# Kernel tuning notes

Measured on AMD Instinct MI355X. Metric: run time of the kernel, lower is better.

The kernel has to match this reference:

```python
import jax, jax.numpy as jnp
import numpy as np

TAU_RC = 0.02
TAU_REF = 0.002
V_TH = 1.0
EPS = 1e-7


def lif_rate(I):
    # LIF firing-rate nonlinearity: r = 1/(tau_ref - tau_rc*log1p(-v_th/I)) for I > v_th+eps else 0
    good = I > V_TH + EPS
    safe_I = jnp.where(good, I, V_TH + 1.0)  # avoid log1p of invalid values
    r = 1.0 / (TAU_REF - TAU_RC * jnp.log1p(-V_TH / safe_I))
    return jnp.where(good, r, 0.0)


def setup_inputs() -> dict:
    key = jax.random.key(0)
    kq, kk, kv, ke, kg, kb = jax.random.split(key, 6)
    B, H, T, D = 2, 16, 2048, 64
    block_size = 2048
    Q = jax.random.normal(kq, (B, H, T, D), dtype=jnp.float32)
    K = jax.random.normal(kk, (B, H, T, D), dtype=jnp.float32)
    V = jax.random.normal(kv, (B, H, T, D), dtype=jnp.float32)
    enc = jax.random.normal(ke, (H, block_size, D), dtype=jnp.float32)
    # F.normalize(enc, dim=-1, eps=1e-8): x / max(||x||, eps)
    norm = jnp.maximum(jnp.linalg.norm(enc, axis=-1, keepdims=True), 1e-8)
    enc_hat = enc / norm
    gain = jax.random.uniform(kg, (1, H, block_size, 1), dtype=jnp.float32) * 200.0
    bias = jax.random.uniform(kb, (1, H, block_size, 1), dtype=jnp.float32)
    return {"Q": Q, "K": K, "V": V, "enc_hat": enc_hat, "gain": gain, "bias": bias}


def reference(Q, K, V, enc_hat, gain, bias):
    B, H, T, D = Q.shape
    temperature = jnp.asarray(D ** 0.5, dtype=Q.dtype)
    E = enc_hat[:, :T, :]          # [H, T, D]
    G = gain[:, :, :T, :]          # [1, H, T, 1]
    BIAS = bias[:, :, :T, :]       # [1, H, T, 1]
    # scores against fixed encoders (K is unused, matching the original module)
    I = G * jnp.einsum('bhtd,hsd->bhts', Q, E) + BIAS   # [B, H, T, T]
    scores = lif_rate(I) / temperature
    causal = jnp.tril(jnp.ones((T, T), dtype=bool))[None, None]
    scores = jnp.where(causal, scores, -jnp.inf)
    attn = jax.nn.softmax(scores, axis=-1)
    return jnp.einsum('bhts,bhsd->bhtd', attn, V)
```

## Files before the change

### kernel.cpp

```cpp
#include <hip/hip_runtime.h>
#include <hip/hip_bf16.h>
#include <math.h>

constexpr int Bb = 2, Hh = 16, Tt = 2048;

typedef __attribute__((ext_vector_type(8))) _Float16 f16x8;
typedef __attribute__((ext_vector_type(8))) short bf16x8;
typedef __attribute__((ext_vector_type(4))) float f32x4;
typedef __attribute__((ext_vector_type(16))) float f32x16;
typedef __attribute__((ext_vector_type(4))) short short4v;
typedef unsigned int u32;

__device__ __forceinline__ short f2bf(float x){ __hip_bfloat16 h = __float2bfloat16(x); return *(short*)&h; }
__device__ __forceinline__ float bf2f(short s){
  u32 u = ((u32)(unsigned short)s) << 16; float f; __builtin_memcpy(&f, &u, 4); return f;
}
__device__ __forceinline__ int swze(int row, int e){ return row*64 + ((((e>>3) ^ (row&7))<<3) | (e&7)); }
__device__ __forceinline__ int swzg(int row, int e0){ return row*64 + ((((e0>>3) ^ (row&7))<<3)); }

__device__ __forceinline__ void gll16(const void* g, void* l){
  __builtin_amdgcn_global_load_lds((const __attribute__((address_space(1))) u32*)g,
                                   (__attribute__((address_space(3))) u32*)l, 16, 0, 0);
}

__global__ __launch_bounds__(256) void prep_e(const float* __restrict__ E, char* __restrict__ Eimg){
  const int hh = blockIdx.x >> 5, j = blockIdx.x & 31;
  const float* src = E + ((size_t)hh * Tt + j * 64) * 64;
  char* dst = Eimg + (size_t)blockIdx.x * 16384;
#pragma unroll
  for (int i = 0; i < 2; ++i) {
    const int gid = threadIdx.x + 256 * i;
    const int row = gid >> 3, gc = gid & 7;
    const float* s8 = src + row * 64 + gc * 8;
    float4 a = *(const float4*)s8;
    float4 c = *(const float4*)(s8 + 4);
    float v[8] = {a.x, a.y, a.z, a.w, c.x, c.y, c.z, c.w};
    f16x8 hv, lv;
#pragma unroll
    for (int k = 0; k < 8; ++k) {
      _Float16 hi = (_Float16)v[k];
      hv[k] = hi; lv[k] = (_Float16)(v[k] - (float)hi);
    }
    const int off = row * 128 + ((gc ^ (row & 7)) << 4);
    *(f16x8*)(dst + off) = hv;
    *(f16x8*)(dst + 8192 + off) = lv;
  }
}

__global__ __launch_bounds__(256) void prep_v(const float* __restrict__ V, char* __restrict__ Vimg){
  __shared__ __align__(16) short Tl[64 * 64];
  const int tid = threadIdx.x;
  const int j = blockIdx.x & 31, bh = blockIdx.x >> 5;
  const int s0 = j * 64;
  {
    const int r = tid >> 2, c0 = (tid & 3) * 16;
    const float* src = V + ((size_t)bh * Tt + s0 + r) * 64 + c0;
#pragma unroll
    for (int i = 0; i < 4; ++i) {
      float4 t4 = ((const float4*)src)[i];
      float vv[4] = {t4.x, t4.y, t4.z, t4.w};
#pragma unroll
      for (int k = 0; k < 4; ++k) Tl[swze(c0 + 4 * i + k, r)] = f2bf(vv[k]);
    }
  }
  __syncthreads();
  {
    const int d = tid >> 2, sg = (tid & 3) * 16;
    bf16x8 a = *(const bf16x8*)&Tl[swzg(d, sg)];
    bf16x8 b = *(const bf16x8*)&Tl[swzg(d, sg + 8)];
    char* dst = Vimg + (size_t)blockIdx.x * 8192 + d * 128;
    *(bf16x8*)(dst + ((((sg >> 3) + 0) ^ (d & 7)) << 4)) = a;
    *(bf16x8*)(dst + ((((sg >> 3) + 1) ^ (d & 7)) << 4)) = b;
  }
}

__global__ __launch_bounds__(256, 3) void lif_attn5(
    const float* __restrict__ Q, const float* __restrict__ gain, const float* __restrict__ bias,
    const char* __restrict__ Eimg, const char* __restrict__ Vimg, float* __restrict__ out)
{
  __shared__ __align__(16) char Eb[2][16384];
  __shared__ __align__(16) char Vb[8192];
  __shared__ __align__(16) char Pb[8192];
  __shared__ __align__(16) float Ls[128];

  const int tid = threadIdx.x, lane = tid & 63, w = tid >> 6;
  const int l31 = lane & 31, hi2 = lane >> 5;
  const int wr = w >> 1, wc = w & 1;
  const int bh = blockIdx.x & 31, tb = 31 - (blockIdx.x >> 5);
  const int b = bh >> 4, h = bh & 15, t0 = tb * 64;
  const int tg = t0 + 32 * wc + l31;

  const char* etile = Eimg + (size_t)(h * 32) * 16384;
  const char* vtile = Vimg + (size_t)(bh * 32) * 8192;

  f16x8 qh[4], ql[4];
  {
    const float* qp = Q + ((size_t)(b * Hh + h) * Tt + tg) * 64 + 8 * hi2;
#pragma unroll
    for (int kk = 0; kk < 4; ++kk) {
      const float* p0 = qp + 16 * kk;
      float4 a = *(const float4*)p0;
      float4 c = *(const float4*)(p0 + 4);
      float v[8] = {a.x, a.y, a.z, a.w, c.x, c.y, c.z, c.w};
#pragma unroll
      for (int k = 0; k < 8; ++k) {
        _Float16 hi = (_Float16)v[k];
        qh[kk][k] = hi; ql[kk][k] = (_Float16)(v[k] - (float)hi);
      }
    }
  }
  const float gt = gain[h * Tt + tg], bt = bias[h * Tt + tg];

  const int rE = 32 * wr + l31;
  const int eB = rE * 128 + ((hi2 ^ (rE & 7)) << 4);
  const int vB = eB;
  const int tl = 32 * wc + l31;
  const int pB = tl * 128 + ((hi2 ^ (tl & 7)) << 4);
  const int pwB = (tl * 128 + ((tl & 7) << 4) + 8 * hi2) ^ (wr << 6);

  f32x16 oacc = 0.f;
  float lsum = 0.f;

  {
    const char* g = etile + tid * 16; char* l = &Eb[0][0] + tid * 16;
#pragma unroll
    for (int c = 0; c < 4; ++c) gll16(g + c * 4096, l + c * 4096);
    const char* gv = vtile + tid * 16; char* lv2 = &Vb[0] + tid * 16;
#pragma unroll
    for (int c = 0; c < 2; ++c) gll16(gv + c * 4096, lv2 + c * 4096);
  }
  asm volatile("s_waitcnt vmcnt(2)" ::: "memory");
  __builtin_amdgcn_s_barrier();
  asm volatile("" ::: "memory");
  __builtin_amdgcn_sched_barrier(0);

  int cur = 0;
  for (int j = 0;;) {
    const int jn = (j < tb) ? j + 1 : tb;
    {
      const char* g = etile + (size_t)jn * 16384 + tid * 16;
      char* l = &Eb[cur ^ 1][0] + tid * 16;
#pragma unroll
      for (int c = 0; c < 4; ++c) gll16(g + c * 4096, l + c * 4096);
    }
    const char* ec = &Eb[cur][0];
    f32x16 sacc = 0.f;
#pragma unroll
    for (int kk = 0; kk < 4; ++kk) {
      f16x8 eh = *(const f16x8*)(ec + (eB ^ (kk << 5)));
      f16x8 el = *(const f16x8*)(ec + 8192 + (eB ^ (kk << 5)));
      sacc = __builtin_amdgcn_mfma_f32_32x32x16_f16(eh, qh[kk], sacc, 0, 0, 0);
      sacc = __builtin_amdgcn_mfma_f32_32x32x16_f16(el, qh[kk], sacc, 0, 0, 0);
      sacc = __builtin_amdgcn_mfma_f32_32x32x16_f16(eh, ql[kk], sacc, 0, 0, 0);
    }
    const int s0 = j * 64;
#pragma unroll
    for (int rq = 0; rq < 4; ++rq) {
      short4v pb;
#pragma unroll
      for (int rr = 0; rr < 4; ++rr) {
        const int sg = s0 + 32 * wr + 8 * rq + 4 * hi2 + rr;
        const float I = fmaf(gt, sacc[4 * rq + rr], bt);
        const float rcpI = __builtin_amdgcn_rcpf(I);
        const float L2 = __log2f((I - 1.0f) * rcpI);
        const float den = fmaf(-0.013862944f, L2, 0.002f);
        const float rd = __builtin_amdgcn_rcpf(den);
        float p = __expf(fmaf(0.125f, rd, -62.5f));
        p = (I > 1.0f + 1e-7f) ? p : 7.1892351e-28f;
        p = (sg <= tg) ? p : 0.0f;
        const short pv = f2bf(p);
        lsum += bf2f(pv);
        pb[rr] = pv;
      }
      *(short4v*)(&Pb[0] + (pwB ^ (rq << 4))) = pb;
    }
    asm volatile("s_waitcnt vmcnt(4) lgkmcnt(0)" ::: "memory");
    __builtin_amdgcn_s_barrier();
    asm volatile("" ::: "memory");
    __builtin_amdgcn_sched_barrier(0);
#pragma unroll
    for (int kk = 0; kk < 4; ++kk) {
      bf16x8 pa = *(const bf16x8*)(&Pb[0] + (pB ^ (kk << 5)));
      bf16x8 vb = *(const bf16x8*)(&Vb[0] + (vB ^ (kk << 5)));
      oacc = __builtin_amdgcn_mfma_f32_32x32x16_bf16(pa, vb, oacc, 0, 0, 0);
    }
    asm volatile("s_waitcnt vmcnt(0)" ::: "memory");
    __builtin_amdgcn_s_barrier();
    asm volatile("" ::: "memory");
    __builtin_amdgcn_sched_barrier(0);
    if (j == tb) break;
    {
      const char* g = vtile + (size_t)jn * 8192 + tid * 16;
      char* l = &Vb[0] + tid * 16;
#pragma unroll
      for (int c = 0; c < 2; ++c) gll16(g + c * 4096, l + c * 4096);
    }
    cur ^= 1; ++j;
  }

  lsum += __shfl_xor(lsum, 32);
  __syncthreads();
  Ls[wr * 64 + tl] = lsum;
  __syncthreads();
  float* ob = out + ((size_t)(b * Hh + h) * Tt + t0) * 64 + 32 * wr + l31;
#pragma unroll
  for (int rq = 0; rq < 4; ++rq) {
    const int tr = 32 * wc + 8 * rq + 4 * hi2;
    f32x4 la = *(const f32x4*)&Ls[tr];
    f32x4 lb = *(const f32x4*)&Ls[64 + tr];
#pragma unroll
    for (int rr = 0; rr < 4; ++rr) {
      const float linv = __builtin_amdgcn_rcpf(la[rr] + lb[rr]);
      ob[(size_t)(tr + rr) * 64] = oacc[4 * rq + rr] * linv;
    }
  }
}

extern "C" void kernel_launch(void* const* d_in, const int* in_sizes, int n_in,
                              void* d_out, int out_size, void* d_ws, size_t ws_size,
                              hipStream_t stream) {
  const float* Q    = (const float*)d_in[0];
  const float* V    = (const float*)d_in[2];
  const float* E    = (const float*)d_in[3];
  const float* gain = (const float*)d_in[4];
  const float* bias = (const float*)d_in[5];
  float* out = (float*)d_out;

  constexpr size_t EIMG_BYTES = (size_t)Hh * 32 * 16384;
  char* Eimg = (char*)d_ws;
  char* Vimg = (char*)d_ws + EIMG_BYTES;

  prep_e<<<Hh * 32, 256, 0, stream>>>(E, Eimg);
  prep_v<<<Bb * Hh * 32, 256, 0, stream>>>(V, Vimg);
  lif_attn5<<<1024, 256, 0, stream>>>(Q, gain, bias, Eimg, Vimg, out);
}
```

Baseline: 85.95 us.

## Keep P in registers via permlane swap, double-buffer V, split-K PV reduction

The P tile no longer round-trips through shared memory. Scores are packed to bf16 with v_cvt_pk_bf16_f32 and rearranged into MFMA operand layout with v_permlane32_swap, so the P·V MFMA consumes them straight from registers. Each wave now covers all 64 output columns over its own 32-key slice, and the two key-slice halves are summed through LDS in the epilogue. V is double-buffered alongside E, which cuts the barriers per iteration from two to one. The causal mask runs only on the diagonal tile, and the exponential uses exp2 with prescaled constants. In exchange the kernel carries two output accumulators (more register pressure) and does an extra reduction at the end; lsum now sums unrounded p instead of the bf16-rounded values.

```diff
diff --git a/kernel.cpp b/kernel.cpp
--- a/kernel.cpp
+++ b/kernel.cpp
@@ -8,13 +8,10 @@
 typedef __attribute__((ext_vector_type(8))) short bf16x8;
 typedef __attribute__((ext_vector_type(4))) float f32x4;
 typedef __attribute__((ext_vector_type(16))) float f32x16;
-typedef __attribute__((ext_vector_type(4))) short short4v;
+typedef __attribute__((ext_vector_type(4))) unsigned int u32x4;
 typedef unsigned int u32;
 
 __device__ __forceinline__ short f2bf(float x){ __hip_bfloat16 h = __float2bfloat16(x); return *(short*)&h; }
-__device__ __forceinline__ float bf2f(short s){
-  u32 u = ((u32)(unsigned short)s) << 16; float f; __builtin_memcpy(&f, &u, 4); return f;
-}
 __device__ __forceinline__ int swze(int row, int e){ return row*64 + ((((e>>3) ^ (row&7))<<3) | (e&7)); }
 __device__ __forceinline__ int swzg(int row, int e0){ return row*64 + ((((e0>>3) ^ (row&7))<<3)); }
 
@@ -22,10 +19,12 @@
   __builtin_amdgcn_global_load_lds((const __attribute__((address_space(1))) u32*)g,
                                    (__attribute__((address_space(3))) u32*)l, 16, 0, 0);
 }
+__device__ __forceinline__ u32 cvtpk(float lo, float hi){
+  u32 d; asm("v_cvt_pk_bf16_f32 %0, %1, %2" : "=v"(d) : "v"(lo), "v"(hi)); return d;
+}
 
 __global__ __launch_bounds__(256) void prep_e(const float* __restrict__ E, char* __restrict__ Eimg){
-  const int hh = blockIdx.x >> 5, j = blockIdx.x & 31;
-  const float* src = E + ((size_t)hh * Tt + j * 64) * 64;
+  const float* src = E + (size_t)blockIdx.x * 4096;
   char* dst = Eimg + (size_t)blockIdx.x * 16384;
 #pragma unroll
   for (int i = 0; i < 2; ++i) {
@@ -74,18 +73,17 @@
   }
 }
 
-__global__ __launch_bounds__(256, 3) void lif_attn5(
+__global__ __launch_bounds__(256, 3) void lif_attn6(
     const float* __restrict__ Q, const float* __restrict__ gain, const float* __restrict__ bias,
     const char* __restrict__ Eimg, const char* __restrict__ Vimg, float* __restrict__ out)
 {
   __shared__ __align__(16) char Eb[2][16384];
-  __shared__ __align__(16) char Vb[8192];
-  __shared__ __align__(16) char Pb[8192];
-  __shared__ __align__(16) float Ls[128];
-
-  const int tid = threadIdx.x, lane = tid & 63, w = tid >> 6;
+  __shared__ __align__(16) char Vb[2][8192];
+  __shared__ __align__(16) float LsS[128];
+
+  const int tid = threadIdx.x, lane = tid & 63;
   const int l31 = lane & 31, hi2 = lane >> 5;
-  const int wr = w >> 1, wc = w & 1;
+  const int w = tid >> 6, wc = w & 1, wr = w >> 1;
   const int bh = blockIdx.x & 31, tb = 31 - (blockIdx.x >> 5);
   const int b = bh >> 4, h = bh & 15, t0 = tb * 64;
   const int tg = t0 + 32 * wc + l31;
@@ -111,37 +109,35 @@
   }
   const float gt = gain[h * Tt + tg], bt = bias[h * Tt + tg];
 
-  const int rE = 32 * wr + l31;
-  const int eB = rE * 128 + ((hi2 ^ (rE & 7)) << 4);
-  const int vB = eB;
-  const int tl = 32 * wc + l31;
-  const int pB = tl * 128 + ((hi2 ^ (tl & 7)) << 4);
-  const int pwB = (tl * 128 + ((tl & 7) << 4) + 8 * hi2) ^ (wr << 6);
-
-  f32x16 oacc = 0.f;
+  const int rS = 32 * wr + l31;
+  const int eB = rS * 128 + ((hi2 ^ (rS & 7)) << 4);
+  const int vB0 = l31 * 128 + (((4 * wr + hi2) ^ (l31 & 7)) << 4);
+  const int vB1 = (32 + l31) * 128 + (((4 * wr + hi2) ^ (l31 & 7)) << 4);
+
+  f32x16 oacc0 = 0.f, oacc1 = 0.f;
   float lsum = 0.f;
 
   {
-    const char* g = etile + tid * 16; char* l = &Eb[0][0] + tid * 16;
-#pragma unroll
-    for (int c = 0; c < 4; ++c) gll16(g + c * 4096, l + c * 4096);
-    const char* gv = vtile + tid * 16; char* lv2 = &Vb[0] + tid * 16;
-#pragma unroll
-    for (int c = 0; c < 2; ++c) gll16(gv + c * 4096, lv2 + c * 4096);
-  }
-  asm volatile("s_waitcnt vmcnt(2)" ::: "memory");
-  __builtin_amdgcn_s_barrier();
-  asm volatile("" ::: "memory");
-  __builtin_amdgcn_sched_barrier(0);
+    const char* g = etile + tid * 16;
+#pragma unroll
+    for (int c2 = 0; c2 < 4; ++c2) gll16(g + c2 * 4096, &Eb[0][0] + tid * 16 + c2 * 4096);
+    const char* gv = vtile + tid * 16;
+#pragma unroll
+    for (int c2 = 0; c2 < 2; ++c2) gll16(gv + c2 * 4096, &Vb[0][0] + tid * 16 + c2 * 4096);
+  }
+  __syncthreads();
 
   int cur = 0;
-  for (int j = 0;;) {
-    const int jn = (j < tb) ? j + 1 : tb;
-    {
-      const char* g = etile + (size_t)jn * 16384 + tid * 16;
+  for (int j = 0; ; ++j) {
+    if (j < tb) {
+      const char* g = etile + (size_t)(j + 1) * 16384 + tid * 16;
       char* l = &Eb[cur ^ 1][0] + tid * 16;
 #pragma unroll
-      for (int c = 0; c < 4; ++c) gll16(g + c * 4096, l + c * 4096);
+      for (int c2 = 0; c2 < 4; ++c2) gll16(g + c2 * 4096, l + c2 * 4096);
+      const char* gv = vtile + (size_t)(j + 1) * 8192 + tid * 16;
+      char* lv = &Vb[cur ^ 1][0] + tid * 16;
+#pragma unroll
+      for (int c2 = 0; c2 < 2; ++c2) gll16(gv + c2 * 4096, lv + c2 * 4096);
     }
     const char* ec = &Eb[cur][0];
     f32x16 sacc = 0.f;
@@ -153,65 +149,77 @@
       sacc = __builtin_amdgcn_mfma_f32_32x32x16_f16(el, qh[kk], sacc, 0, 0, 0);
       sacc = __builtin_amdgcn_mfma_f32_32x32x16_f16(eh, ql[kk], sacc, 0, 0, 0);
     }
-    const int s0 = j * 64;
+    float p[16];
+#pragma unroll
+    for (int r = 0; r < 16; ++r) {
+      const float I = fmaf(gt, sacc[r], bt);
+      const float L2 = __log2f((I - 1.0f) * __builtin_amdgcn_rcpf(I));
+      const float den = fmaf(-0.013862944f, L2, 0.002f);
+      const float rd = __builtin_amdgcn_rcpf(den);
+      const float pv = __builtin_amdgcn_exp2f(fmaf(0.18033688f, rd, -90.169312f));
+      p[r] = (I > 1.0f + 1e-7f) ? pv : 7.1892351e-28f;
+    }
+    if (j == tb) {
+#pragma unroll
+      for (int rq = 0; rq < 4; ++rq)
+#pragma unroll
+        for (int rr = 0; rr < 4; ++rr)
+          if (32 * wr + 8 * rq + 4 * hi2 + rr > 32 * wc + l31) p[4 * rq + rr] = 0.f;
+    }
+#pragma unroll
+    for (int r = 0; r < 16; ++r) lsum += p[r];
+    const char* vc = &Vb[cur][0];
+#pragma unroll
+    for (int kp = 0; kp < 2; ++kp) {
+      u32 x0 = cvtpk(p[8 * kp + 0], p[8 * kp + 1]);
+      u32 x1 = cvtpk(p[8 * kp + 2], p[8 * kp + 3]);
+      u32 y0 = cvtpk(p[8 * kp + 4], p[8 * kp + 5]);
+      u32 y1 = cvtpk(p[8 * kp + 6], p[8 * kp + 7]);
+      asm("v_permlane32_swap_b32 %0, %1" : "+v"(x0), "+v"(y0));
+      asm("v_permlane32_swap_b32 %0, %1" : "+v"(x1), "+v"(y1));
+      u32x4 af = {x0, x1, y0, y1};
+      bf16x8 pa = *(bf16x8*)&af;
+      bf16x8 vb0 = *(const bf16x8*)(vc + (vB0 ^ (kp << 5)));
+      bf16x8 vb1 = *(const bf16x8*)(vc + (vB1 ^ (kp << 5)));
+      oacc0 = __builtin_amdgcn_mfma_f32_32x32x16_bf16(pa, vb0, oacc0, 0, 0, 0);
+      oacc1 = __builtin_amdgcn_mfma_f32_32x32x16_bf16(pa, vb1, oacc1, 0, 0, 0);
+    }
+    if (j == tb) break;
+    __syncthreads();
+    cur ^= 1;
+  }
+
+  lsum += __shfl_xor(lsum, 32);
+  if (lane < 32) LsS[wr * 64 + wc * 32 + l31] = lsum;
+  __syncthreads();
+  float* red = (float*)&Eb[0][0];
+  if (wr == 1) {
+#pragma unroll
+    for (int rq = 0; rq < 4; ++rq)
+#pragma unroll
+      for (int rr = 0; rr < 4; ++rr) {
+        const int tr = 8 * rq + 4 * hi2 + rr;
+        red[wc * 2048 + tr * 64 + l31]      = oacc0[4 * rq + rr];
+        red[wc * 2048 + tr * 64 + 32 + l31] = oacc1[4 * rq + rr];
+      }
+  }
+  __syncthreads();
+  if (wr == 0) {
+    float* ob = out + ((size_t)(b * Hh + h) * Tt + t0 + 32 * wc) * 64;
 #pragma unroll
     for (int rq = 0; rq < 4; ++rq) {
-      short4v pb;
+      const int tr0 = 8 * rq + 4 * hi2;
+      f32x4 lt0 = *(const f32x4*)&LsS[wc * 32 + tr0];
+      f32x4 lt1 = *(const f32x4*)&LsS[64 + wc * 32 + tr0];
 #pragma unroll
       for (int rr = 0; rr < 4; ++rr) {
-        const int sg = s0 + 32 * wr + 8 * rq + 4 * hi2 + rr;
-        const float I = fmaf(gt, sacc[4 * rq + rr], bt);
-        const float rcpI = __builtin_amdgcn_rcpf(I);
-        const float L2 = __log2f((I - 1.0f) * rcpI);
-        const float den = fmaf(-0.013862944f, L2, 0.002f);
-        const float rd = __builtin_amdgcn_rcpf(den);
-        float p = __expf(fmaf(0.125f, rd, -62.5f));
-        p = (I > 1.0f + 1e-7f) ? p : 7.1892351e-28f;
-        p = (sg <= tg) ? p : 0.0f;
-        const short pv = f2bf(p);
-        lsum += bf2f(pv);
-        pb[rr] = pv;
+        const int tr = tr0 + rr;
+        const float linv = __builtin_amdgcn_rcpf(lt0[rr] + lt1[rr]);
+        const float o0 = oacc0[4 * rq + rr] + red[wc * 2048 + tr * 64 + l31];
+        const float o1 = oacc1[4 * rq + rr] + red[wc * 2048 + tr * 64 + 32 + l31];
+        ob[(size_t)tr * 64 + l31]      = o0 * linv;
+        ob[(size_t)tr * 64 + 32 + l31] = o1 * linv;
       }
-      *(short4v*)(&Pb[0] + (pwB ^ (rq << 4))) = pb;
-    }
-    asm volatile("s_waitcnt vmcnt(4) lgkmcnt(0)" ::: "memory");
-    __builtin_amdgcn_s_barrier();
-    asm volatile("" ::: "memory");
-    __builtin_amdgcn_sched_barrier(0);
-#pragma unroll
-    for (int kk = 0; kk < 4; ++kk) {
-      bf16x8 pa = *(const bf16x8*)(&Pb[0] + (pB ^ (kk << 5)));
-      bf16x8 vb = *(const bf16x8*)(&Vb[0] + (vB ^ (kk << 5)));
-      oacc = __builtin_amdgcn_mfma_f32_32x32x16_bf16(pa, vb, oacc, 0, 0, 0);
-    }
-    asm volatile("s_waitcnt vmcnt(0)" ::: "memory");
-    __builtin_amdgcn_s_barrier();
-    asm volatile("" ::: "memory");
-    __builtin_amdgcn_sched_barrier(0);
-    if (j == tb) break;
-    {
-      const char* g = vtile + (size_t)jn * 8192 + tid * 16;
-      char* l = &Vb[0] + tid * 16;
-#pragma unroll
-      for (int c = 0; c < 2; ++c) gll16(g + c * 4096, l + c * 4096);
-    }
-    cur ^= 1; ++j;
-  }
-
-  lsum += __shfl_xor(lsum, 32);
-  __syncthreads();
-  Ls[wr * 64 + tl] = lsum;
-  __syncthreads();
-  float* ob = out + ((size_t)(b * Hh + h) * Tt + t0) * 64 + 32 * wr + l31;
-#pragma unroll
-  for (int rq = 0; rq < 4; ++rq) {
-    const int tr = 32 * wc + 8 * rq + 4 * hi2;
-    f32x4 la = *(const f32x4*)&Ls[tr];
-    f32x4 lb = *(const f32x4*)&Ls[64 + tr];
-#pragma unroll
-    for (int rr = 0; rr < 4; ++rr) {
-      const float linv = __builtin_amdgcn_rcpf(la[rr] + lb[rr]);
-      ob[(size_t)(tr + rr) * 64] = oacc[4 * rq + rr] * linv;
     }
   }
 }
@@ -232,5 +240,5 @@
 
   prep_e<<<Hh * 32, 256, 0, stream>>>(E, Eimg);
   prep_v<<<Bb * Hh * 32, 256, 0, stream>>>(V, Vimg);
-  lif_attn5<<<1024, 256, 0, stream>>>(Q, gain, bias, Eimg, Vimg, out);
-}
+  lif_attn6<<<1024, 256, 0, stream>>>(Q, gain, bias, Eimg, Vimg, out);
+}
```

Result: faster. 79.36 us (-7.7%).
